# Kernel tuning notes

Hardware: AMD Instinct MI355X
Metric: run time of the kernel (lower is better)

## Reference

```python
import jax, jax.numpy as jnp
import numpy as np

D = 256      # d_model
H = 8        # n_heads
HD = D // H  # head_dim = 32
P = 16       # point dim per head


def setup_inputs() -> dict:
    key = jax.random.key(0)
    ks = jax.random.split(key, 12)
    B, S = 2, 2048
    w = lambda k, shape: jax.random.normal(k, shape, jnp.float32) * 0.02
    return {
        "seq_repr": jax.random.normal(ks[0], (B, S, D), jnp.float32),
        "coords": jax.random.normal(ks[1], (B, S, 3, 3), jnp.float32),
        "frames": jax.random.normal(ks[2], (B, S, 4), jnp.float32),
        "mask": jnp.ones((B, S), jnp.int32),
        "Wq": w(ks[3], (D, D)), "bq": jnp.zeros((D,), jnp.float32),
        "Wk": w(ks[4], (D, D)), "bk": jnp.zeros((D,), jnp.float32),
        "Wv": w(ks[5], (D, D)), "bv": jnp.zeros((D,), jnp.float32),
        "Wpq": w(ks[6], (3, H * P)), "bpq": jnp.zeros((H * P,), jnp.float32),
        "Wpk": w(ks[7], (3, H * P)), "bpk": jnp.zeros((H * P,), jnp.float32),
        "Wo": w(ks[8], (D, D)), "bo": jnp.zeros((D,), jnp.float32),
        "Wpo": w(ks[9], (H * P, 3)), "bpo": jnp.zeros((3,), jnp.float32),
        "attn_bias": jnp.zeros((H,), jnp.float32),
    }


def reference(seq_repr, coords, frames, mask, Wq, bq, Wk, bk, Wv, bv,
              Wpq, bpq, Wpk, bpk, Wo, bo, Wpo, bpo, attn_bias):
    B, S, _ = seq_repr.shape
    q = (seq_repr @ Wq + bq).reshape(B, S, H, HD)
    k = (seq_repr @ Wk + bk).reshape(B, S, H, HD)
    v = (seq_repr @ Wv + bv).reshape(B, S, H, HD)

    rep = coords[..., 1, :]                                  # [B,S,3] representative atom
    pq = (rep @ Wpq + bpq).reshape(B, S, H, P)
    pk = (rep @ Wpk + bpk).reshape(B, S, H, P)

    scale = 1.0 / np.sqrt(HD)
    scores = (jnp.einsum('bihd,bjhd->bhij', q, k) * scale
              + jnp.einsum('bihp,bjhp->bhij', pq, pk) * 0.25  # 1/sqrt(16)
              + attn_bias[None, :, None, None])

    mask2d = (mask[:, :, None] * mask[:, None, :])[:, None]  # [B,1,S,S]
    scores = jnp.where(mask2d == 0, jnp.float32(-1e9), scores)

    w = jax.nn.softmax(scores, axis=-1)                      # [B,H,S,S]

    seq_ctx = jnp.einsum('bhij,bjhd->bihd', w, v).reshape(B, S, D)
    pt_ctx = jnp.einsum('bhij,bjhp->bihp', w, pq).reshape(B, S, H * P)

    seq_out = seq_ctx @ Wo + bo                              # [B,S,D]
    point_out = pt_ctx @ Wpo + bpo                           # [B,S,3]
    return (seq_out, point_out)
```

## Files before the change

### kernel.cpp

```cpp
#include <hip/hip_runtime.h>
#include <hip/hip_bf16.h>

#define D_ 256
#define H_ 8
#define B_ 2
#define S_ 2048
#define MTOT 4096
#define AUGQ 64
#define NBH 16
#define KPAD 72
#define NSPLIT 4
#define NJ 8
#define LOG2E 1.4426950408889634f

typedef __attribute__((ext_vector_type(8))) short short8;
typedef __attribute__((ext_vector_type(4))) short short4v;
typedef __attribute__((ext_vector_type(4))) float f32x4;

static __device__ __forceinline__ short bf16_of(float f) {
  union { __hip_bfloat16 h; short s; } u;
  u.h = __float2bfloat16(f);
  return u.s;
}
static __device__ __forceinline__ float f_of_bf16(short s) {
  union { float f; unsigned int u; } u;
  u.u = ((unsigned int)(unsigned short)s) << 16;
  return u.f;
}

static __device__ __forceinline__ int sinv64(int c) {
  return (((((c >> 2) & 1) << 1) | ((c >> 5) & 1)) << 4) + (((c >> 3) & 3) << 2) + (c & 3);
}


__global__ void prep_all(const float* __restrict__ Wq, const float* __restrict__ Wk,
                         const float* __restrict__ Wv, const float* __restrict__ Wo,
                         const float* __restrict__ coords, const int* __restrict__ mask,
                         const float* __restrict__ Wpq, const float* __restrict__ bpq,
                         const float* __restrict__ Wpk, const float* __restrict__ bpk,
                         short* __restrict__ Wqkv_t, short* __restrict__ Wo_t,
                         short* __restrict__ Qa, short* __restrict__ Ka,
                         short* __restrict__ VaT) {
  int gid = blockIdx.x * 256 + threadIdx.x;
  int NT = gridDim.x * 256;
  for (int idx = gid; idx < 768 * 256; idx += NT) {
    int n = idx >> 8, k = idx & 255;
    const float* W = (n < 256) ? Wq : (n < 512 ? Wk : Wv);
    Wqkv_t[idx] = bf16_of(W[k * 256 + (n & 255)]);
  }
  for (int idx = gid; idx < 256 * 256; idx += NT) {
    int n = idx >> 8, k = idx & 255;
    Wo_t[idx] = bf16_of(Wo[k * 256 + n]);
  }
  for (int idx = gid; idx < MTOT * 8; idx += NT) {
    int m = idx >> 3, h = idx & 7;
    int b = m >> 11, s = m & 2047;
    float r0 = coords[m * 9 + 3], r1 = coords[m * 9 + 4], r2 = coords[m * 9 + 5];
    size_t base = ((size_t)(b * 8 + h) * S_ + s) * AUGQ;
    short8 pqv[2], pkv[2];
#pragma unroll
    for (int c = 0; c < 2; c++)
#pragma unroll
      for (int i = 0; i < 8; i++) {
        int j = h * 16 + c * 8 + i;
        float pq = r0 * Wpq[j] + r1 * Wpq[128 + j] + r2 * Wpq[256 + j] + bpq[j];
        float pk = r0 * Wpk[j] + r1 * Wpk[128 + j] + r2 * Wpk[256 + j] + bpk[j];
        pqv[c][i] = bf16_of(pq * LOG2E);
        pkv[c][i] = bf16_of(pk * 0.25f);
      }
    short8 padq = {};
    padq[0] = bf16_of(LOG2E);
    short8 padk = {};
    padk[0] = mask[m] ? (short)0 : bf16_of(-1e9f);
    short8 z = {};
    *reinterpret_cast<short8*>(&Qa[base + 32]) = pqv[0];
    *reinterpret_cast<short8*>(&Qa[base + 40]) = pqv[1];
    *reinterpret_cast<short8*>(&Qa[base + 48]) = padq;
    *reinterpret_cast<short8*>(&Qa[base + 56]) = z;
    *reinterpret_cast<short8*>(&Ka[base + 32]) = pkv[0];
    *reinterpret_cast<short8*>(&Ka[base + 40]) = pkv[1];
    *reinterpret_cast<short8*>(&Ka[base + 48]) = padk;
    *reinterpret_cast<short8*>(&Ka[base + 56]) = z;
  }
  for (int idx = gid; idx < NBH * 16 * (S_ / 8); idx += NT) {
    int s8 = idx & 255, p = (idx >> 8) & 15, bh = idx >> 12;
    int b = bh >> 3, h = bh & 7, j = h * 16 + p;
    float w0 = Wpq[j], w1 = Wpq[128 + j], w2 = Wpq[256 + j], bb = bpq[j];
    short8 o;
#pragma unroll
    for (int i = 0; i < 8; i++) {
      int c = (s8 & 7) * 8 + i;
      int m = b * 2048 + (s8 >> 3) * 64 + sinv64(c);
      o[i] = bf16_of(coords[m * 9 + 3] * w0 + coords[m * 9 + 4] * w1 +
                     coords[m * 9 + 5] * w2 + bb);
    }
    *reinterpret_cast<short8*>(&VaT[((size_t)bh * 48 + 32 + p) * S_ + s8 * 8]) = o;
  }
}


__global__ __launch_bounds__(256) void qkv_gemm(
    const float* __restrict__ X, const short* __restrict__ Wt,
    const float* __restrict__ bq, const float* __restrict__ bk, const float* __restrict__ bv,
    short* __restrict__ Qa, short* __restrict__ Ka, short* __restrict__ VaT) {
  __shared__ __align__(16) short As[64 * 136];
  __shared__ __align__(16) short Bs[64 * 136];
  int m0 = blockIdx.x * 64, n0 = blockIdx.y * 64;
  int tid = threadIdx.x, lane = tid & 63, w = tid >> 6;
  int t = lane & 15, g = lane >> 4, kf = g * 8;
  int wr = (w >> 1) * 32, wc = (w & 1) * 32;
  f32x4 acc[2][2] = {};
  int srow = tid >> 2, skc = (tid & 3) * 32;
  for (int ph = 0; ph < 2; ph++) {
    int k0 = ph * 128;
    __syncthreads();
    {
      const float* xs = &X[(size_t)(m0 + srow) * 256 + k0 + skc];
      short4v av[8];
#pragma unroll
      for (int i = 0; i < 8; i++) {
        f32x4 xv = *reinterpret_cast<const f32x4*>(&xs[i * 4]);
        short4v o;
        o[0] = bf16_of(xv[0]); o[1] = bf16_of(xv[1]);
        o[2] = bf16_of(xv[2]); o[3] = bf16_of(xv[3]);
        av[i] = o;
      }
#pragma unroll
      for (int i = 0; i < 8; i++)
        *reinterpret_cast<short4v*>(&As[srow * 136 + skc + i * 4]) = av[i];
      const uint4* wsrc = reinterpret_cast<const uint4*>(&Wt[(size_t)(n0 + srow) * 256 + k0 + skc]);
#pragma unroll
      for (int i = 0; i < 4; i++)
        *reinterpret_cast<uint4*>(&Bs[srow * 136 + skc + i * 8]) = wsrc[i];
    }
    __syncthreads();
#pragma unroll
    for (int kk = 0; kk < 4; kk++) {
      short8 a[2], bb[2];
#pragma unroll
      for (int i = 0; i < 2; i++)
        a[i] = *reinterpret_cast<const short8*>(&As[(wr + i * 16 + t) * 136 + kk * 32 + kf]);
#pragma unroll
      for (int jj = 0; jj < 2; jj++)
        bb[jj] = *reinterpret_cast<const short8*>(&Bs[(wc + jj * 16 + t) * 136 + kk * 32 + kf]);
#pragma unroll
      for (int i = 0; i < 2; i++)
#pragma unroll
        for (int jj = 0; jj < 2; jj++)
          acc[i][jj] = __builtin_amdgcn_mfma_f32_16x16x32_bf16(a[i], bb[jj], acc[i][jj], 0, 0, 0);
    }
  }
  __syncthreads();
  short* Cs = As;
  const float scale = 0.17677669529663687f * LOG2E;
  int b = m0 >> 11, sbase = m0 & 2047;
#pragma unroll
  for (int i = 0; i < 2; i++)
#pragma unroll
    for (int jj = 0; jj < 2; jj++)
#pragma unroll
      for (int r = 0; r < 4; r++) {
        int rl = wr + i * 16 + g * 4 + r;
        int cl = wc + jj * 16 + t;
        int n = n0 + cl;
        float v = acc[i][jj][r];
        if (n < 256) v = (v + bq[n]) * scale;
        else if (n < 512) v = v + bk[n - 256];
        else v = v + bv[n - 512];
        Cs[rl * 72 + cl] = bf16_of(v);
      }
  __syncthreads();
  if (n0 < 512) {
#pragma unroll
    for (int i2 = 0; i2 < 2; i2++) {
      int task = tid + i2 * 256;
      int row = task >> 3, c = task & 7;
      int n = n0 + c * 8;
      short* dst = (n < 256) ? Qa : Ka;
      int nn = n & 255;
      int hh = nn >> 5, d = nn & 31;
      *reinterpret_cast<short8*>(&dst[((size_t)(b * 8 + hh) * S_ + sbase + row) * AUGQ + d]) =
          *reinterpret_cast<const short8*>(&Cs[row * 72 + c * 8]);
    }
  } else {
    int hv0 = (n0 - 512) >> 5;
#pragma unroll
    for (int i2 = 0; i2 < 2; i2++) {
      int task = tid + i2 * 256;
      int fl = task >> 3, s8 = task & 7;
      short8 o;
#pragma unroll
      for (int i = 0; i < 8; i++) o[i] = Cs[sinv64(s8 * 8 + i) * 72 + fl];
      int hh = hv0 + (fl >> 5), d = fl & 31;
      *reinterpret_cast<short8*>(&VaT[((size_t)(b * 8 + hh) * 48 + d) * S_ + sbase + s8 * 8]) = o;
    }
  }
}


__global__ __launch_bounds__(256, 4) void attn(
    const short* __restrict__ Qa, const short* __restrict__ Ka,
    const short* __restrict__ VaT,
    short* __restrict__ Ctx, float* __restrict__ AccL) {
  __shared__ __align__(16) char smem[32256];

  int bid = blockIdx.x;
  int xcd = bid & 7, slot = bid >> 3;
  int gidx = xcd * 8 + (slot >> 4);
  int it = slot & 15;
  int split = gidx & 3;
  int bhv = gidx >> 2;

  int tid = threadIdx.x, lane = tid & 63, w = tid >> 6;
  int t = lane & 15, g = lane >> 4, kf = g * 8;
  int q0w = it * 128 + w * 32;
  size_t bh = (size_t)bhv * S_;

  short8 aq[2][2];
#pragma unroll
  for (int g2 = 0; g2 < 2; g2++)
#pragma unroll
    for (int c = 0; c < 2; c++)
      aq[g2][c] = *reinterpret_cast<const short8*>(
          &Qa[(bh + q0w + g2 * 16 + t) * AUGQ + c * 32 + kf]);

  f32x4 OaccA[3] = {}, OaccB[3] = {};
  float lsum0 = 0.f, lsum1 = 0.f;

  uint4 kreg0, kreg1, vreg0, vreg1;
  int srow = tid >> 3, sko = (tid & 7) * 8;
  const int jt0 = split * NJ;

  auto issue = [&](int jt) {
    const uint4* ks = reinterpret_cast<const uint4*>(&Ka[(bh + jt * 64) * AUGQ]);
    kreg0 = ks[tid];
    kreg1 = ks[tid + 256];
    size_t vb = (size_t)bhv * 48 * S_ + jt * 64;
    vreg0 = *reinterpret_cast<const uint4*>(&VaT[vb + (size_t)srow * S_ + sko]);
    if (tid < 128)
      vreg1 = *reinterpret_cast<const uint4*>(&VaT[vb + (size_t)(srow + 32) * S_ + sko]);
  };
  auto commit = [&](int buf) {
    short* Kd = (short*)(smem + buf * 9216);
    short* Vd = (short*)(smem + 18432 + buf * 6912);
    *reinterpret_cast<uint4*>(&Kd[srow * KPAD + sko]) = kreg0;
    *reinterpret_cast<uint4*>(&Kd[(srow + 32) * KPAD + sko]) = kreg1;
    *reinterpret_cast<uint4*>(&Vd[srow * KPAD + sko]) = vreg0;
    if (tid < 128)
      *reinterpret_cast<uint4*>(&Vd[(srow + 32) * KPAD + sko]) = vreg1;
  };

  issue(jt0);
  commit(0);
  __syncthreads();

  for (int j = 0; j < NJ; j++) {
    int cur = j & 1;
    if (j + 1 < NJ) issue(jt0 + j + 1);
    const short* Kc = (const short*)(smem + cur * 9216);
    const short* Vc = (const short*)(smem + 18432 + cur * 6912);
    short8 pA[2], pB[2];
#pragma unroll
    for (int sub = 0; sub < 4; sub++) {
      short8 ka0 = *reinterpret_cast<const short8*>(&Kc[(sub * 16 + t) * KPAD + kf]);
      short8 ka1 = *reinterpret_cast<const short8*>(&Kc[(sub * 16 + t) * KPAD + 32 + kf]);
      f32x4 sA = {}, sB = {};
      sA = __builtin_amdgcn_mfma_f32_16x16x32_bf16(ka0, aq[0][0], sA, 0, 0, 0);
      sA = __builtin_amdgcn_mfma_f32_16x16x32_bf16(ka1, aq[0][1], sA, 0, 0, 0);
      sB = __builtin_amdgcn_mfma_f32_16x16x32_bf16(ka0, aq[1][0], sB, 0, 0, 0);
      sB = __builtin_amdgcn_mfma_f32_16x16x32_bf16(ka1, aq[1][1], sB, 0, 0, 0);
      float a0 = exp2f(sA[0]), a1 = exp2f(sA[1]), a2 = exp2f(sA[2]), a3 = exp2f(sA[3]);
      float b0 = exp2f(sB[0]), b1 = exp2f(sB[1]), b2 = exp2f(sB[2]), b3 = exp2f(sB[3]);
      lsum0 += (a0 + a1) + (a2 + a3);
      lsum1 += (b0 + b1) + (b2 + b3);
      int ww = sub & 1, off = (sub >> 1) * 4;
      pA[ww][off + 0] = bf16_of(a0); pA[ww][off + 1] = bf16_of(a1);
      pA[ww][off + 2] = bf16_of(a2); pA[ww][off + 3] = bf16_of(a3);
      pB[ww][off + 0] = bf16_of(b0); pB[ww][off + 1] = bf16_of(b1);
      pB[ww][off + 2] = bf16_of(b2); pB[ww][off + 3] = bf16_of(b3);
    }
    __builtin_amdgcn_s_setprio(1);
#pragma unroll
    for (int tt = 0; tt < 3; tt++) {
#pragma unroll
      for (int w2 = 0; w2 < 2; w2++) {
        short8 va = *reinterpret_cast<const short8*>(&Vc[(tt * 16 + t) * KPAD + w2 * 32 + kf]);
        OaccA[tt] = __builtin_amdgcn_mfma_f32_16x16x32_bf16(va, pA[w2], OaccA[tt], 0, 0, 0);
        OaccB[tt] = __builtin_amdgcn_mfma_f32_16x16x32_bf16(va, pB[w2], OaccB[tt], 0, 0, 0);
      }
    }
    __builtin_amdgcn_s_setprio(0);
    if (j + 1 < NJ) commit(cur ^ 1);
    __syncthreads();
  }

  lsum0 += __shfl_xor(lsum0, 16); lsum0 += __shfl_xor(lsum0, 32);
  lsum1 += __shfl_xor(lsum1, 16); lsum1 += __shfl_xor(lsum1, 32);

  float* Of = (float*)smem;
#pragma unroll
  for (int tt = 0; tt < 3; tt++)
#pragma unroll
    for (int r = 0; r < 4; r++) {
      Of[(w * 32 + t) * 52 + tt * 16 + g * 4 + r] = OaccA[tt][r];
      Of[(w * 32 + 16 + t) * 52 + tt * 16 + g * 4 + r] = OaccB[tt][r];
    }
  if (lane < 16) {
    size_t lb = (size_t)(split * NBH + bhv) * S_ + q0w + lane;
    AccL[lb] = lsum0;
    AccL[lb + 16] = lsum1;
  }
  __syncthreads();
  short* CtxP = Ctx + (size_t)split * NBH * S_ * 48;
  size_t obase = bh + it * 128;
  for (int task = tid; task < 768; task += 256) {
    int row = task / 6, c8 = task % 6;
    const float* src = &Of[row * 52 + c8 * 8];
    short8 o;
#pragma unroll
    for (int i = 0; i < 8; i++) o[i] = bf16_of(src[i]);
    *reinterpret_cast<short8*>(&CtxP[(obase + row) * 48 + c8 * 8]) = o;
  }
}


__global__ __launch_bounds__(512) void out_gemm(
    const short* __restrict__ Ctx, const float* __restrict__ AccL,
    const short* __restrict__ Wot, const float* __restrict__ bo,
    const float* __restrict__ Wpo, const float* __restrict__ bpo,
    float* __restrict__ Out) {
  const size_t CTXSZ = (size_t)NBH * S_ * 48;
  int m0 = blockIdx.x * 64;
  int tid = threadIdx.x;
  int b = m0 >> 11, sbase = m0 & 2047;

  if (blockIdx.y == 4) {
    int row = tid >> 3, hh = tid & 7;
    int m = m0 + row, s = sbase + row;
    size_t rowO = (size_t)(b * 8 + hh) * S_ + s;
    float l = 0.f;
#pragma unroll
    for (int sp = 0; sp < NSPLIT; sp++) l += AccL[(size_t)sp * NBH * S_ + rowO];
    float inv = 1.0f / l;
    float a0 = 0.f, a1 = 0.f, a2 = 0.f;
#pragma unroll
    for (int half = 0; half < 2; half++) {
      float sum[8] = {};
#pragma unroll
      for (int sp = 0; sp < NSPLIT; sp++) {
        short8 v = *reinterpret_cast<const short8*>(&Ctx[sp * CTXSZ + rowO * 48 + 32 + half * 8]);
#pragma unroll
        for (int c = 0; c < 8; c++) sum[c] += f_of_bf16(v[c]);
      }
#pragma unroll
      for (int c = 0; c < 8; c++) {
        float val = sum[c] * inv;
        int j = hh * 16 + half * 8 + c;
        a0 += val * Wpo[j * 3 + 0];
        a1 += val * Wpo[j * 3 + 1];
        a2 += val * Wpo[j * 3 + 2];
      }
    }
    a0 += __shfl_xor(a0, 1); a0 += __shfl_xor(a0, 2); a0 += __shfl_xor(a0, 4);
    a1 += __shfl_xor(a1, 1); a1 += __shfl_xor(a1, 2); a1 += __shfl_xor(a1, 4);
    a2 += __shfl_xor(a2, 1); a2 += __shfl_xor(a2, 2); a2 += __shfl_xor(a2, 4);
    if (hh == 0) {
      float* po = Out + (size_t)MTOT * 256;
      po[(size_t)m * 3 + 0] = a0 + bpo[0];
      po[(size_t)m * 3 + 1] = a1 + bpo[1];
      po[(size_t)m * 3 + 2] = a2 + bpo[2];
    }
    return;
  }

  __shared__ __align__(16) short As[64 * 136];
  __shared__ __align__(16) short Bs[64 * 136];
  int n0 = blockIdx.y * 64;
  int lane = tid & 63, w = tid >> 6;
  int t = lane & 15, g = lane >> 4, kf = g * 8;
  int wm = w & 3, wn = w >> 2;
  f32x4 acc[2] = {};
  int srow = tid >> 3, skc = (tid & 7) * 16;
  for (int ph = 0; ph < 2; ph++) {
    int k0 = ph * 128;
    __syncthreads();
    {
      int kg = k0 + skc;
      int hh = kg >> 5, d0 = kg & 31;
      size_t rowO = (size_t)(b * 8 + hh) * S_ + sbase + srow;
      float l = 0.f;
#pragma unroll
      for (int sp = 0; sp < NSPLIT; sp++) l += AccL[(size_t)sp * NBH * S_ + rowO];
      float inv = 1.0f / l;
#pragma unroll
      for (int half = 0; half < 2; half++) {
        float sum[8] = {};
#pragma unroll
        for (int sp = 0; sp < NSPLIT; sp++) {
          short8 a = *reinterpret_cast<const short8*>(&Ctx[sp * CTXSZ + rowO * 48 + d0 + half * 8]);
#pragma unroll
          for (int c = 0; c < 8; c++) sum[c] += f_of_bf16(a[c]);
        }
        short8 o;
#pragma unroll
        for (int c = 0; c < 8; c++) o[c] = bf16_of(sum[c] * inv);
        *reinterpret_cast<short8*>(&As[srow * 136 + skc + half * 8]) = o;
      }
      *reinterpret_cast<uint4*>(&Bs[srow * 136 + skc]) =
          *reinterpret_cast<const uint4*>(&Wot[(size_t)(n0 + srow) * 256 + kg]);
      *reinterpret_cast<uint4*>(&Bs[srow * 136 + skc + 8]) =
          *reinterpret_cast<const uint4*>(&Wot[(size_t)(n0 + srow) * 256 + kg + 8]);
    }
    __syncthreads();
#pragma unroll
    for (int kk = 0; kk < 4; kk++) {
      short8 a = *reinterpret_cast<const short8*>(&As[(wm * 16 + t) * 136 + kk * 32 + kf]);
#pragma unroll
      for (int jj = 0; jj < 2; jj++) {
        short8 bb = *reinterpret_cast<const short8*>(&Bs[(wn * 32 + jj * 16 + t) * 136 + kk * 32 + kf]);
        acc[jj] = __builtin_amdgcn_mfma_f32_16x16x32_bf16(a, bb, acc[jj], 0, 0, 0);
      }
    }
  }
#pragma unroll
  for (int jj = 0; jj < 2; jj++)
#pragma unroll
    for (int r = 0; r < 4; r++) {
      int mrow = m0 + wm * 16 + g * 4 + r;
      int n = n0 + wn * 32 + jj * 16 + t;
      Out[(size_t)mrow * 256 + n] = acc[jj][r] + bo[n];
    }
}


extern "C" void kernel_launch(void* const* d_in, const int* in_sizes, int n_in,
                              void* d_out, int out_size, void* d_ws, size_t ws_size,
                              hipStream_t stream) {
  const float* seq    = (const float*)d_in[0];
  const float* coords = (const float*)d_in[1];
  const int*   mask   = (const int*)d_in[3];
  const float* Wq  = (const float*)d_in[4];
  const float* bq  = (const float*)d_in[5];
  const float* Wk  = (const float*)d_in[6];
  const float* bk  = (const float*)d_in[7];
  const float* Wv  = (const float*)d_in[8];
  const float* bv  = (const float*)d_in[9];
  const float* Wpq = (const float*)d_in[10];
  const float* bpq = (const float*)d_in[11];
  const float* Wpk = (const float*)d_in[12];
  const float* bpk = (const float*)d_in[13];
  const float* Wo  = (const float*)d_in[14];
  const float* bo  = (const float*)d_in[15];
  const float* Wpo = (const float*)d_in[16];
  const float* bpo = (const float*)d_in[17];
  float* out = (float*)d_out;

  char* ws = (char*)d_ws;
  short* Wqkv_t = (short*)ws; ws += 768 * 256 * 2;
  short* Wo_t   = (short*)ws; ws += 256 * 256 * 2;
  short* Qa     = (short*)ws; ws += (size_t)NBH * S_ * AUGQ * 2;
  short* Ka     = (short*)ws; ws += (size_t)NBH * S_ * AUGQ * 2;
  short* VaT    = (short*)ws; ws += (size_t)NBH * 48 * S_ * 2;
  short* Ctx    = (short*)ws; ws += (size_t)NSPLIT * NBH * S_ * 48 * 2;
  float* AccL   = (float*)ws; ws += (size_t)NSPLIT * NBH * S_ * 4;

  prep_all<<<1024, 256, 0, stream>>>(Wq, Wk, Wv, Wo, coords, mask, Wpq, bpq, Wpk, bpk,
                                     Wqkv_t, Wo_t, Qa, Ka, VaT);
  qkv_gemm<<<dim3(64, 12), 256, 0, stream>>>(seq, Wqkv_t, bq, bk, bv, Qa, Ka, VaT);
  attn<<<1024, 256, 0, stream>>>(Qa, Ka, VaT, Ctx, AccL);
  out_gemm<<<dim3(64, 5), 512, 0, stream>>>(Ctx, AccL, Wo_t, bo, Wpo, bpo, out);
}
```

Measured before the change: 65.76 us.

## Pre-convert activations to bf16 in prep kernel and tile weight transposes via LDS

The prep kernel is restructured into block-specialized roles. Weight transposes now go through a shared-memory tile so reads and writes are coalesced, where before each thread did a strided gather. The fp32 seq_repr is converted to bf16 once into a new workspace buffer, and qkv_gemm now loads that bf16 data directly instead of reading fp32 and converting it in every N-tile block (12 times). This saves redundant fp32 reads and conversions, at the cost of one extra bf16 write and read round trip through global memory.

```diff
diff --git a/kernel.cpp b/kernel.cpp
--- a/kernel.cpp
+++ b/kernel.cpp
@@ -33,26 +33,69 @@
 }
 
 
-__global__ void prep_all(const float* __restrict__ Wq, const float* __restrict__ Wk,
-                         const float* __restrict__ Wv, const float* __restrict__ Wo,
-                         const float* __restrict__ coords, const int* __restrict__ mask,
-                         const float* __restrict__ Wpq, const float* __restrict__ bpq,
-                         const float* __restrict__ Wpk, const float* __restrict__ bpk,
-                         short* __restrict__ Wqkv_t, short* __restrict__ Wo_t,
-                         short* __restrict__ Qa, short* __restrict__ Ka,
-                         short* __restrict__ VaT) {
-  int gid = blockIdx.x * 256 + threadIdx.x;
-  int NT = gridDim.x * 256;
-  for (int idx = gid; idx < 768 * 256; idx += NT) {
-    int n = idx >> 8, k = idx & 255;
-    const float* W = (n < 256) ? Wq : (n < 512 ? Wk : Wv);
-    Wqkv_t[idx] = bf16_of(W[k * 256 + (n & 255)]);
-  }
-  for (int idx = gid; idx < 256 * 256; idx += NT) {
-    int n = idx >> 8, k = idx & 255;
-    Wo_t[idx] = bf16_of(Wo[k * 256 + n]);
-  }
-  for (int idx = gid; idx < MTOT * 8; idx += NT) {
+__global__ __launch_bounds__(256) void prep_all(
+    const float* __restrict__ Wq, const float* __restrict__ Wk,
+    const float* __restrict__ Wv, const float* __restrict__ Wo,
+    const float* __restrict__ X, const float* __restrict__ coords,
+    const int* __restrict__ mask,
+    const float* __restrict__ Wpq, const float* __restrict__ bpq,
+    const float* __restrict__ Wpk, const float* __restrict__ bpk,
+    short* __restrict__ Wqkv_t, short* __restrict__ Wo_t,
+    short* __restrict__ Xb,
+    short* __restrict__ Qa, short* __restrict__ Ka, short* __restrict__ VaT) {
+  int bid = blockIdx.x, tid = threadIdx.x;
+
+  if (bid < 64) {
+    __shared__ short T[64][72];
+    const float* src;
+    short* dst;
+    int k0, n0g;
+    if (bid < 48) {
+      int nt = bid >> 2;
+      k0 = (bid & 3) * 64;
+      n0g = nt * 64;
+      src = (n0g < 256) ? Wq : (n0g < 512 ? Wk : Wv);
+      dst = Wqkv_t;
+    } else {
+      int t2 = bid - 48;
+      k0 = (t2 & 3) * 64;
+      n0g = (t2 >> 2) * 64;
+      src = Wo;
+      dst = Wo_t;
+    }
+    int ncol = n0g & 255;
+    int rr = tid >> 4, cc = (tid & 15) * 4;
+#pragma unroll
+    for (int i = 0; i < 4; i++) {
+      int r = rr + i * 16;
+      f32x4 v = *reinterpret_cast<const f32x4*>(&src[(size_t)(k0 + r) * 256 + ncol + cc]);
+      T[cc + 0][r] = bf16_of(v[0]);
+      T[cc + 1][r] = bf16_of(v[1]);
+      T[cc + 2][r] = bf16_of(v[2]);
+      T[cc + 3][r] = bf16_of(v[3]);
+    }
+    __syncthreads();
+    int n = tid >> 2, kk = (tid & 3) * 16;
+    *reinterpret_cast<short8*>(&dst[(size_t)(n0g + n) * 256 + k0 + kk]) =
+        *reinterpret_cast<const short8*>(&T[n][kk]);
+    *reinterpret_cast<short8*>(&dst[(size_t)(n0g + n) * 256 + k0 + kk + 8]) =
+        *reinterpret_cast<const short8*>(&T[n][kk + 8]);
+    return;
+  }
+
+  if (bid < 576) {
+    size_t i = (size_t)(bid - 64) * 2048 + tid * 8;
+    f32x4 v0 = *reinterpret_cast<const f32x4*>(&X[i]);
+    f32x4 v1 = *reinterpret_cast<const f32x4*>(&X[i + 4]);
+    short8 o;
+    o[0] = bf16_of(v0[0]); o[1] = bf16_of(v0[1]); o[2] = bf16_of(v0[2]); o[3] = bf16_of(v0[3]);
+    o[4] = bf16_of(v1[0]); o[5] = bf16_of(v1[1]); o[6] = bf16_of(v1[2]); o[7] = bf16_of(v1[3]);
+    *reinterpret_cast<short8*>(&Xb[i]) = o;
+    return;
+  }
+
+  if (bid < 704) {
+    int idx = (bid - 576) * 256 + tid;
     int m = idx >> 3, h = idx & 7;
     int b = m >> 11, s = m & 2047;
     float r0 = coords[m * 9 + 3], r1 = coords[m * 9 + 4], r2 = coords[m * 9 + 5];
@@ -81,8 +124,11 @@
     *reinterpret_cast<short8*>(&Ka[base + 40]) = pkv[1];
     *reinterpret_cast<short8*>(&Ka[base + 48]) = padk;
     *reinterpret_cast<short8*>(&Ka[base + 56]) = z;
-  }
-  for (int idx = gid; idx < NBH * 16 * (S_ / 8); idx += NT) {
+    return;
+  }
+
+  {
+    int idx = (bid - 704) * 256 + tid;
     int s8 = idx & 255, p = (idx >> 8) & 15, bh = idx >> 12;
     int b = bh >> 3, h = bh & 7, j = h * 16 + p;
     float w0 = Wpq[j], w1 = Wpq[128 + j], w2 = Wpq[256 + j], bb = bpq[j];
@@ -100,7 +146,7 @@
 
 
 __global__ __launch_bounds__(256) void qkv_gemm(
-    const float* __restrict__ X, const short* __restrict__ Wt,
+    const short* __restrict__ Xb, const short* __restrict__ Wt,
     const float* __restrict__ bq, const float* __restrict__ bk, const float* __restrict__ bv,
     short* __restrict__ Qa, short* __restrict__ Ka, short* __restrict__ VaT) {
   __shared__ __align__(16) short As[64 * 136];
@@ -115,20 +161,11 @@
     int k0 = ph * 128;
     __syncthreads();
     {
-      const float* xs = &X[(size_t)(m0 + srow) * 256 + k0 + skc];
-      short4v av[8];
-#pragma unroll
-      for (int i = 0; i < 8; i++) {
-        f32x4 xv = *reinterpret_cast<const f32x4*>(&xs[i * 4]);
-        short4v o;
-        o[0] = bf16_of(xv[0]); o[1] = bf16_of(xv[1]);
-        o[2] = bf16_of(xv[2]); o[3] = bf16_of(xv[3]);
-        av[i] = o;
-      }
-#pragma unroll
-      for (int i = 0; i < 8; i++)
-        *reinterpret_cast<short4v*>(&As[srow * 136 + skc + i * 4]) = av[i];
+      const uint4* xsrc = reinterpret_cast<const uint4*>(&Xb[(size_t)(m0 + srow) * 256 + k0 + skc]);
       const uint4* wsrc = reinterpret_cast<const uint4*>(&Wt[(size_t)(n0 + srow) * 256 + k0 + skc]);
+#pragma unroll
+      for (int i = 0; i < 4; i++)
+        *reinterpret_cast<uint4*>(&As[srow * 136 + skc + i * 8]) = xsrc[i];
 #pragma unroll
       for (int i = 0; i < 4; i++)
         *reinterpret_cast<uint4*>(&Bs[srow * 136 + skc + i * 8]) = wsrc[i];
@@ -458,15 +495,17 @@
   char* ws = (char*)d_ws;
   short* Wqkv_t = (short*)ws; ws += 768 * 256 * 2;
   short* Wo_t   = (short*)ws; ws += 256 * 256 * 2;
+  short* Xb     = (short*)ws; ws += (size_t)MTOT * D_ * 2;
   short* Qa     = (short*)ws; ws += (size_t)NBH * S_ * AUGQ * 2;
   short* Ka     = (short*)ws; ws += (size_t)NBH * S_ * AUGQ * 2;
   short* VaT    = (short*)ws; ws += (size_t)NBH * 48 * S_ * 2;
   short* Ctx    = (short*)ws; ws += (size_t)NSPLIT * NBH * S_ * 48 * 2;
   float* AccL   = (float*)ws; ws += (size_t)NSPLIT * NBH * S_ * 4;
 
-  prep_all<<<1024, 256, 0, stream>>>(Wq, Wk, Wv, Wo, coords, mask, Wpq, bpq, Wpk, bpk,
-                                     Wqkv_t, Wo_t, Qa, Ka, VaT);
-  qkv_gemm<<<dim3(64, 12), 256, 0, stream>>>(seq, Wqkv_t, bq, bk, bv, Qa, Ka, VaT);
+  prep_all<<<960, 256, 0, stream>>>(Wq, Wk, Wv, Wo, seq, coords, mask,
+                                    Wpq, bpq, Wpk, bpk,
+                                    Wqkv_t, Wo_t, Xb, Qa, Ka, VaT);
+  qkv_gemm<<<dim3(64, 12), 256, 0, stream>>>(Xb, Wqkv_t, bq, bk, bv, Qa, Ka, VaT);
   attn<<<1024, 256, 0, stream>>>(Qa, Ka, VaT, Ctx, AccL);
   out_gemm<<<dim3(64, 5), 512, 0, stream>>>(Ctx, AccL, Wo_t, bo, Wpo, bpo, out);
 }
```

Result: faster. 60.21 us (-8.4%).
